# Kernel tuning notes

Hardware: AMD Instinct MI355X
Metric: run time of the kernel (lower is better)

Reference implementation:

```python
import jax, jax.numpy as jnp
import numpy as np
import math

N, DIM, HEADS = 4096, 128, 8
HC = DIM // HEADS      # MHA per-head dim = 16
GC = DIM               # TransformerConv per-head out_channels = dim (concat=False)
E = 65536
FFN = 2048
EPS = 1e-5

def layernorm(x, g, b):
    m = x.mean(-1, keepdims=True)
    v = ((x - m) ** 2).mean(-1, keepdims=True)
    return (x - m) * jax.lax.rsqrt(v + EPS) * g + b

def setup_inputs() -> dict:
    key = jax.random.key(0)
    ks = jax.random.split(key, 24)
    s = 0.02
    def nrm(k, shape):
        return jax.random.normal(k, shape, jnp.float32) * s
    return dict(
        x=jax.random.normal(ks[0], (N, DIM), jnp.float32),
        edge_index=jax.random.randint(ks[1], (2, E), 0, N),
        edge_attr=jax.random.normal(ks[2], (E, DIM), jnp.float32),
        n1_g=jnp.ones((DIM,)), n1_b=jnp.zeros((DIM,)),
        n2_g=jnp.ones((DIM,)), n2_b=jnp.zeros((DIM,)),
        n3_g=jnp.ones((DIM,)), n3_b=jnp.zeros((DIM,)),
        w_qkv=nrm(ks[3], (DIM, 3 * DIM)), b_qkv=jnp.zeros((3 * DIM,)),
        w_o=nrm(ks[4], (DIM, DIM)), b_o=jnp.zeros((DIM,)),
        w_query=nrm(ks[5], (DIM, HEADS * GC)), b_query=jnp.zeros((HEADS * GC,)),
        w_key=nrm(ks[6], (DIM, HEADS * GC)), b_key=jnp.zeros((HEADS * GC,)),
        w_value=nrm(ks[7], (DIM, HEADS * GC)), b_value=jnp.zeros((HEADS * GC,)),
        w_edge=nrm(ks[8], (DIM, HEADS * GC)), b_edge=jnp.zeros((HEADS * GC,)),
        w_skip=nrm(ks[9], (DIM, GC)), b_skip=jnp.zeros((GC,)),
        w_beta=nrm(ks[10], (3 * GC, 1)),
        w_f1=nrm(ks[11], (DIM, FFN)), b_f1=jnp.zeros((FFN,)),
        w_f2=nrm(ks[12], (FFN, DIM)), b_f2=jnp.zeros((DIM,)),
        w_dyn=nrm(ks[13], (2 * DIM, DIM)), b_dyn=jnp.zeros((DIM,)),
    )

def reference(x, edge_index, edge_attr, n1_g, n1_b, n2_g, n2_b, n3_g, n3_b,
              w_qkv, b_qkv, w_o, b_o,
              w_query, b_query, w_key, b_key, w_value, b_value,
              w_edge, b_edge, w_skip, b_skip, w_beta,
              w_f1, b_f1, w_f2, b_f2, w_dyn, b_dyn):
    residual = x
    xn = layernorm(x, n1_g, n1_b)
    # ---- dense self-attention (batch 1, batch_first MHA, eval mode) ----
    qkv = xn @ w_qkv + b_qkv
    q, k, v = jnp.split(qkv, 3, axis=-1)
    q = q.reshape(N, HEADS, HC)
    k = k.reshape(N, HEADS, HC)
    v = v.reshape(N, HEADS, HC)
    scores = jnp.einsum('qhd,khd->hqk', q, k) / math.sqrt(HC)
    probs = jax.nn.softmax(scores, axis=-1)
    attn = jnp.einsum('hqk,khd->qhd', probs, v).reshape(N, DIM)
    attn = attn @ w_o + b_o
    x = residual + attn
    # ---- TransformerConv (heads=8, concat=False -> mean, beta=True, edge_dim=dim) ----
    xn2 = layernorm(x, n2_g, n2_b)
    src, dst = edge_index[0], edge_index[1]   # source -> target flow
    qg = (xn2 @ w_query + b_query).reshape(N, HEADS, GC)
    kg = (xn2 @ w_key + b_key).reshape(N, HEADS, GC)
    vg = (xn2 @ w_value + b_value).reshape(N, HEADS, GC)
    eg = (edge_attr @ w_edge + b_edge).reshape(E, HEADS, GC)
    kj = kg[src] + eg                          # key_j + edge embedding
    alpha = jnp.einsum('ehd,ehd->eh', qg[dst], kj) / math.sqrt(GC)  # [E,H]
    amax = jax.ops.segment_max(alpha, dst, num_segments=N)          # [N,H]
    amax = jnp.where(jnp.isfinite(amax), amax, 0.0)
    ea = jnp.exp(alpha - amax[dst])
    denom = jax.ops.segment_sum(ea, dst, num_segments=N)
    w = ea / (denom[dst] + 1e-16)              # segment softmax per target node
    msg = (vg[src] + eg) * w[:, :, None]       # value_j + edge, scaled
    agg = jax.ops.segment_sum(msg, dst, num_segments=N)  # [N,H,GC]
    out = agg.mean(axis=1)                     # concat=False -> head mean
    x_r = xn2 @ w_skip + b_skip                # root/skip path
    beta = jax.nn.sigmoid(jnp.concatenate([out, x_r, out - x_r], axis=-1) @ w_beta)
    graph_out = beta * x_r + (1.0 - beta) * out
    x = x + graph_out
    # ---- FFN ----
    xn3 = layernorm(x, n3_g, n3_b)
    ffn = jax.nn.gelu(xn3 @ w_f1 + b_f1, approximate=False) @ w_f2 + b_f2
    x = x + ffn
    # ---- gated residual fusion ----
    gate = jax.nn.sigmoid(jnp.concatenate([x, residual], axis=-1) @ w_dyn + b_dyn)
    return x * gate + residual * (1.0 - gate)
```

## Files before the change

### kernel.cpp

```cpp
#include <hip/hip_runtime.h>
#include <math.h>
#include <cstddef>

#define NN 4096
#define DIMC 128
#define NHEADS 8
#define NE 65536

typedef unsigned short ushort_t;
typedef short bs8 __attribute__((ext_vector_type(8)));
typedef float f32x16 __attribute__((ext_vector_type(16)));
typedef _Float16 h4 __attribute__((ext_vector_type(4)));
typedef __fp16 fp16x2 __attribute__((ext_vector_type(2)));
typedef float f4t __attribute__((ext_vector_type(4)));

__device__ __forceinline__ float b2f(ushort_t u){
  unsigned int i = ((unsigned int)u)<<16; float f;
  __builtin_memcpy(&f,&i,4); return f;
}
__device__ __forceinline__ ushort_t f2b(float f){
  unsigned int x; __builtin_memcpy(&x,&f,4);
  unsigned int r = x + 0x7fffu + ((x>>16)&1u);
  return (ushort_t)(r>>16);
}
__device__ __forceinline__ float bdot8(uint4 a, uint4 b){
  unsigned int ua[4]={a.x,a.y,a.z,a.w}, ub[4]={b.x,b.y,b.z,b.w};
  float s=0.f;
  #pragma unroll
  for (int i=0;i<4;++i){
    unsigned int al=ua[i]<<16, ah=ua[i]&0xffff0000u, bl=ub[i]<<16, bh=ub[i]&0xffff0000u;
    float fa,fb,fc,fd;
    __builtin_memcpy(&fa,&al,4); __builtin_memcpy(&fb,&ah,4);
    __builtin_memcpy(&fc,&bl,4); __builtin_memcpy(&fd,&bh,4);
    s += fa*fc + fb*fd;
  }
  return s;
}
__device__ __forceinline__ float bfdot8v(uint4 a, float4 e0, float4 e1){
  unsigned int ua[4]={a.x,a.y,a.z,a.w};
  float eb[8]={e0.x,e0.y,e0.z,e0.w,e1.x,e1.y,e1.z,e1.w};
  float s=0.f;
  #pragma unroll
  for (int i=0;i<4;++i){
    unsigned int al=ua[i]<<16, ah=ua[i]&0xffff0000u;
    float fa,fb;
    __builtin_memcpy(&fa,&al,4); __builtin_memcpy(&fb,&ah,4);
    s += fa*eb[2*i] + fb*eb[2*i+1];
  }
  return s;
}

__device__ void scan256(const int* __restrict__ cnt, int* __restrict__ rows,
                        int* __restrict__ cursor){
  __shared__ int sums[256];
  int t = threadIdx.x;
  int base = t*16;
  int c[16]; int local=0;
  #pragma unroll
  for (int i=0;i<16;++i){ c[i]=cnt[base+i]; local+=c[i]; }
  sums[t]=local; __syncthreads();
  for (int off=1; off<256; off<<=1){
    int v = (t>=off)? sums[t-off] : 0; __syncthreads();
    sums[t]+=v; __syncthreads();
  }
  int r = sums[t]-local;
  #pragma unroll
  for (int i=0;i<16;++i){ rows[base+i]=r; cursor[base+i]=r; r+=c[i]; }
  if (t==255) rows[4096]=r;
}

__global__ __launch_bounds__(256) void ln_kernel(const float* __restrict__ x,
    const float* __restrict__ g, const float* __restrict__ b, ushort_t* __restrict__ y,
    const int* __restrict__ ei, int* __restrict__ cnt,
    int* __restrict__ cursor, int* __restrict__ csr,
    int* __restrict__ pack, int* __restrict__ packe){
  int bb = blockIdx.x;
  if (bb >= 1024){
    int e = (bb-1024)*256 + threadIdx.x;
    int src = ei[e] & (NN-1), dst = ei[NE+e] & (NN-1);
    int pos = atomicAdd(&cursor[dst],1);
    if (pos >= 0 && pos < NE){
      csr[pos]=e; pack[pos]=src|(dst<<12); packe[pos]=e|(src<<16);
    }
    return;
  }
  int n = bb*4 + (threadIdx.x>>6);
  int l = threadIdx.x & 63;
  int d0 = 2*l;
  float2 v = *(const float2*)&x[(size_t)n*DIMC + d0];
  float s = v.x+v.y;
  s += __shfl_xor(s,1); s += __shfl_xor(s,2); s += __shfl_xor(s,4);
  s += __shfl_xor(s,8); s += __shfl_xor(s,16); s += __shfl_xor(s,32);
  float mean = s*(1.0f/128.0f);
  float c0=v.x-mean, c1=v.y-mean;
  float q=c0*c0+c1*c1;
  q += __shfl_xor(q,1); q += __shfl_xor(q,2); q += __shfl_xor(q,4);
  q += __shfl_xor(q,8); q += __shfl_xor(q,16); q += __shfl_xor(q,32);
  float rinv = rsqrtf(q*(1.0f/128.0f)+1e-5f);
  float2 gv = *(const float2*)&g[d0];
  float2 bv = *(const float2*)&b[d0];
  unsigned int pk = ((unsigned int)f2b(c1*rinv*gv.y+bv.y)<<16) | (unsigned int)f2b(c0*rinv*gv.x+bv.x);
  *(unsigned int*)&y[(size_t)n*DIMC + d0] = pk;
  if (cnt){
    int gid = bb*256 + threadIdx.x;
    if (gid < NE) atomicAdd(&cnt[ei[NE+gid] & (NN-1)],1);
  }
}

#define QSCALE 0.36067376022224085f
__global__ __launch_bounds__(256) void megawcvt_kernel(
    const float* __restrict__ w_qkv, const float* __restrict__ w_o,
    const float* __restrict__ w_q, const float* __restrict__ w_k,
    const float* __restrict__ w_v, const float* __restrict__ w_e,
    const float* __restrict__ w_f1, const float* __restrict__ w_f2,
    const float* __restrict__ bq, const float* __restrict__ bk,
    const float* __restrict__ w_dyn, const float* __restrict__ b_qkv,
    ushort_t* __restrict__ WBqkv, ushort_t* __restrict__ WBo, ushort_t* __restrict__ WBG,
    ushort_t* __restrict__ WETB, ushort_t* __restrict__ WBf1, ushort_t* __restrict__ WBf2,
    ushort_t* __restrict__ WCAT, float* __restrict__ BCAT, ushort_t* __restrict__ WDYN,
    int* __restrict__ COUNT, float* __restrict__ BQKV)
{
  int b = blockIdx.x, tid = threadIdx.x;
  if (b < 1216){
    const float* src; int srcStride; ushort_t* dst; int dstStride;
    int n0, k0; float scale = 1.0f;
    if (b < 48){ int nt=b>>2, kt=b&3; src=w_qkv; srcStride=384; dst=WBqkv; dstStride=128;
      n0=nt*32; k0=kt*32; if (nt<4) scale=QSCALE; }
    else if (b < 64){ int l=b-48, nt=l>>2, kt=l&3; src=w_o; srcStride=128; dst=WBo; dstStride=128; n0=nt*32; k0=kt*32; }
    else if (b < 192){ int l=b-64, nt=l>>2, kt=l&3; src=w_q; srcStride=1024; dst=WBG; dstStride=128; n0=nt*32; k0=kt*32; }
    else if (b < 320){ int l=b-192, nt=l>>2, kt=l&3; src=w_k; srcStride=1024; dst=WBG+1024*128; dstStride=128; n0=nt*32; k0=kt*32; }
    else if (b < 448){ int l=b-320, nt=l>>2, kt=l&3; src=w_e; srcStride=1024; dst=WETB; dstStride=128; n0=nt*32; k0=kt*32; }
    else if (b < 704){ int l=b-448, nt=l>>2, kt=l&3; src=w_f1; srcStride=2048; dst=WBf1; dstStride=128; n0=nt*32; k0=kt*32; }
    else if (b < 960){ int l=b-704, nt=l>>6, kt=l&63; src=w_f2; srcStride=128; dst=WBf2; dstStride=2048; n0=nt*32; k0=kt*32; }
    else if (b < 1088){ int l=b-960, h=l>>4, tt=l&15, nt=tt>>2, kt=tt&3;
      src=w_v+h*128; srcStride=1024; dst=WCAT+h*128; dstStride=2048; n0=nt*32; k0=kt*32; scale=0.125f; }
    else { int l=b-1088, h=l>>4, tt=l&15, nt=tt>>2, kt=tt&3;
      src=w_e+h*128; srcStride=1024; dst=WCAT+1024+h*128; dstStride=2048; n0=nt*32; k0=kt*32; scale=0.125f; }
    __shared__ float lt[32*33];
    int rr = tid>>3, cg = (tid&7)*4;
    float4 v = *(const float4*)&src[(size_t)(k0+rr)*srcStride + n0 + cg];
    lt[rr*33+cg]=v.x; lt[rr*33+cg+1]=v.y; lt[rr*33+cg+2]=v.z; lt[rr*33+cg+3]=v.w;
    __syncthreads();
    ushort_t o[4] __attribute__((aligned(8)));
    #pragma unroll
    for (int j=0;j<4;++j) o[j] = f2b(lt[(cg+j)*33 + rr]*scale);
    *(ushort4*)&dst[(size_t)(n0+rr)*dstStride + k0 + cg] = *(ushort4*)o;
  } else {
    for (int id=(b-1216)*256+tid; id<39296; id += 40*256){
      if (id < 2048) BCAT[id] = (id<1024)? bq[id] : bk[id-1024];
      else if (id < 34816){ int l=id-2048; WDYN[l]=f2b(w_dyn[l]); }
      else if (id < 38912) COUNT[id-34816]=0;
      else { int l=id-38912; BQKV[l]=b_qkv[l]*((l<128)?QSCALE:1.0f); }
    }
  }
}

template<int A_BF16, int C_MODE, int FUSE_SCAN>
__global__ __launch_bounds__(256) void mgemm_kernel(
    const void* __restrict__ Av, int lda, int strideA,
    const ushort_t* __restrict__ BT, int ldbt, int strideB,
    const float* __restrict__ bias,
    const float* __restrict__ res,
    void* __restrict__ Cv, int ldc, int strideC,
    int K, int act_gelu, _Float16* __restrict__ vtout,
    const int* __restrict__ scnt, int* __restrict__ srows, int* __restrict__ scur)
{
  if (FUSE_SCAN){
    if (blockIdx.x == gridDim.x-1){
      if (blockIdx.y==0 && blockIdx.z==0) scan256(scnt, srows, scur);
      return;
    }
  }
  int z = blockIdx.z;
  int m0 = blockIdx.y*128, n0 = blockIdx.x*64;
  int tid = threadIdx.x;
  int w = tid>>6, lane = tid&63;
  int kg = lane>>5;
  int ml = w*32 + (lane&31);
  int sw = (ml>>1)&3;
  __shared__ ushort_t As[128*32];
  const ushort_t* BTz = BT + (size_t)z*strideB;
  f32x16 acc[2];
  #pragma unroll
  for (int i=0;i<16;++i){ acc[0][i]=0.f; acc[1][i]=0.f; }

  for (int k0=0; k0<K; k0+=32){
    {
      int rr = tid>>1, kc = (tid&1)*16;
      int rowg = m0 + rr;
      ushort_t tmp[16] __attribute__((aligned(16)));
      if (A_BF16){
        const ushort_t* A = (const ushort_t*)Av + (size_t)z*strideA;
        uint4 u0 = *(const uint4*)&A[(size_t)rowg*lda + k0 + kc];
        uint4 u1 = *(const uint4*)&A[(size_t)rowg*lda + k0 + kc + 8];
        __builtin_memcpy(tmp, &u0, 16); __builtin_memcpy(tmp+8, &u1, 16);
      } else {
        const float* A = (const float*)Av + (size_t)z*strideA;
        const float* p = &A[(size_t)rowg*lda + k0 + kc];
        float4 f0=*(const float4*)p, f1=*(const float4*)(p+4);
        float4 f2v=*(const float4*)(p+8), f3=*(const float4*)(p+12);
        tmp[0]=f2b(f0.x); tmp[1]=f2b(f0.y); tmp[2]=f2b(f0.z); tmp[3]=f2b(f0.w);
        tmp[4]=f2b(f1.x); tmp[5]=f2b(f1.y); tmp[6]=f2b(f1.z); tmp[7]=f2b(f1.w);
        tmp[8]=f2b(f2v.x); tmp[9]=f2b(f2v.y); tmp[10]=f2b(f2v.z); tmp[11]=f2b(f2v.w);
        tmp[12]=f2b(f3.x); tmp[13]=f2b(f3.y); tmp[14]=f2b(f3.z); tmp[15]=f2b(f3.w);
      }
      int swr = (rr>>1)&3, c0 = kc>>3;
      *(uint4*)&As[rr*32 + (((c0  )^swr)*8)] = *(const uint4*)tmp;
      *(uint4*)&As[rr*32 + (((c0+1)^swr)*8)] = *(const uint4*)(tmp+8);
    }
    __syncthreads();
    bs8 a0 = *(bs8*)&As[ml*32 + (((0*2+kg)^sw)*8)];
    bs8 a1 = *(bs8*)&As[ml*32 + (((1*2+kg)^sw)*8)];
    #pragma unroll
    for (int nt=0; nt<2; ++nt){
      const ushort_t* bp = &BTz[(size_t)(n0 + nt*32 + (lane&31))*ldbt + k0 + kg*8];
      uint4 rb0 = *(const uint4*)bp;
      uint4 rb1 = *(const uint4*)(bp + 16);
      bs8 b0, b1;
      __builtin_memcpy(&b0, &rb0, 16); __builtin_memcpy(&b1, &rb1, 16);
      acc[nt] = __builtin_amdgcn_mfma_f32_32x32x16_bf16(a0, b0, acc[nt], 0,0,0);
      acc[nt] = __builtin_amdgcn_mfma_f32_32x32x16_bf16(a1, b1, acc[nt], 0,0,0);
    }
    __syncthreads();
  }
  #pragma unroll
  for (int nt=0; nt<2; ++nt){
    int col = n0 + nt*32 + (lane&31);
    float bv = bias ? bias[col] : 0.f;
    #pragma unroll
    for (int r=0; r<16; ++r){
      int rowl = (r&3) + 8*(r>>2) + 4*kg;
      int row = m0 + w*32 + rowl;
      float v = acc[nt][r] + bv;
      if (act_gelu) v = 0.5f*v*(1.0f+erff(v*0.70710678118654752f));
      if (res) v += res[(size_t)row*ldc + col];
      size_t idx = (size_t)z*strideC + (size_t)row*ldc + col;
      if (C_MODE==1)      ((ushort_t*)Cv)[idx] = f2b(v);
      else if (C_MODE==2){
        _Float16 hv = (_Float16)v;
        ((_Float16*)Cv)[idx] = hv;
        if (vtout && col>=256) vtout[(size_t)(col-256)*4096 + row] = hv;
      }
      else                ((float*)Cv)[idx]    = v;
    }
  }
}

__global__ __launch_bounds__(512) void flash_kernel(const _Float16* __restrict__ qkvh,
    const _Float16* __restrict__ vt, float* __restrict__ attn){
  int h = blockIdx.y;
  int w = threadIdx.x >> 6, lane = threadIdx.x & 63;
  int q0 = blockIdx.x*64;
  int col = lane & 15, quad = lane >> 4;
  __shared__ float ll[8][4][16];
  __shared__ float lo[8][4][256];
  h4 qf[4];
  #pragma unroll
  for (int t=0;t<4;++t)
    qf[t] = *(const h4*)&qkvh[(size_t)(q0+t*16+col)*384 + h*16 + quad*4];
  f4t ov[4];
  float ls[4] = {0.f,0.f,0.f,0.f};
  #pragma unroll
  for (int t=0;t<4;++t){ ov[t][0]=0.f; ov[t][1]=0.f; ov[t][2]=0.f; ov[t][3]=0.f; }
  const _Float16* kbase = qkvh + 128 + h*16 + quad*4;
  const _Float16* vbase = vt + (size_t)(h*16+col)*4096 + quad*4;
  int jbeg = w*512, jend = jbeg + 512;
  h4 kf = *(const h4*)&kbase[(size_t)(jbeg+col)*384];
  h4 vf = *(const h4*)&vbase[jbeg];
  for (int j0=jbeg; j0<jend; j0+=16){
    h4 kc=kf, vc=vf;
    if (j0+16<jend){
      kf = *(const h4*)&kbase[(size_t)(j0+16+col)*384];
      vf = *(const h4*)&vbase[j0+16];
    }
    f4t s[4];
    #pragma unroll
    for (int t=0;t<4;++t){
      s[t][0]=0.f; s[t][1]=0.f; s[t][2]=0.f; s[t][3]=0.f;
      s[t] = __builtin_amdgcn_mfma_f32_16x16x16f16(kc, qf[t], s[t], 0,0,0);
    }
    #pragma unroll
    for (int t=0;t<4;++t){
      float p0=__builtin_amdgcn_exp2f(s[t][0]), p1=__builtin_amdgcn_exp2f(s[t][1]);
      float p2=__builtin_amdgcn_exp2f(s[t][2]), p3=__builtin_amdgcn_exp2f(s[t][3]);
      ls[t] += (p0+p1)+(p2+p3);
      fp16x2 plo = __builtin_amdgcn_cvt_pkrtz(p0,p1);
      fp16x2 phi = __builtin_amdgcn_cvt_pkrtz(p2,p3);
      h4 pf;
      pf[0]=(_Float16)plo[0]; pf[1]=(_Float16)plo[1];
      pf[2]=(_Float16)phi[0]; pf[3]=(_Float16)phi[1];
      ov[t] = __builtin_amdgcn_mfma_f32_16x16x16f16(vc, pf, ov[t], 0,0,0);
    }
  }
  #pragma unroll
  for (int t=0;t<4;++t){
    float l = ls[t];
    l += __shfl_xor(l,16);
    l += __shfl_xor(l,32);
    if (lane<16) ll[w][t][lane]=l;
    *(float4*)&lo[w][t][lane*4] = make_float4(ov[t][0],ov[t][1],ov[t][2],ov[t][3]);
  }
  __syncthreads();
  if (w < 4){
    int t = w;
    float l = 0.f;
    #pragma unroll
    for (int ww=0; ww<8; ++ww) l += ll[ww][t][col];
    float4 os = make_float4(0.f,0.f,0.f,0.f);
    #pragma unroll
    for (int ww=0; ww<8; ++ww){
      float4 owv = *(const float4*)&lo[ww][t][lane*4];
      os.x += owv.x; os.y += owv.y; os.z += owv.z; os.w += owv.w;
    }
    float inv = 1.0f/l;
    *(float4*)&attn[(size_t)(q0+t*16+col)*128 + h*16 + quad*4] =
        make_float4(os.x*inv, os.y*inv, os.z*inv, os.w*inv);
  }
}

__global__ __launch_bounds__(256) void alpha_kernel(
    const float* __restrict__ ea, const ushort_t* __restrict__ qkvsg,
    const ushort_t* __restrict__ t, const int* __restrict__ csr,
    const int* __restrict__ pack, float* __restrict__ alpha){
  int tid = threadIdx.x;
  int w = tid>>6, lane = tid&63;
  int h = lane>>3, li = lane&7;
  int off = h*128 + li*16;
  int ibase = blockIdx.x*8 + w*2;
  int2 pk = *(const int2*)&pack[ibase];
  int2 ec = *(const int2*)&csr[ibase];
  int e0 = ec.x & (NE-1), e1 = ec.y & (NE-1);
  int s0 = pk.x & 4095, d0 = (pk.x>>12) & 4095;
  int s1 = pk.y & 4095, d1 = (pk.y>>12) & 4095;

  const ushort_t* q0p = &qkvsg[(size_t)d0*2048 + off];
  const ushort_t* k0p = &qkvsg[(size_t)s0*2048 + 1024 + off];
  const ushort_t* t0p = &t[(size_t)d0*1024 + off];
  const float*    e0p = &ea[(size_t)e0*128 + li*16];
  const ushort_t* q1p = &qkvsg[(size_t)d1*2048 + off];
  const ushort_t* k1p = &qkvsg[(size_t)s1*2048 + 1024 + off];
  const ushort_t* t1p = &t[(size_t)d1*1024 + off];
  const float*    e1p = &ea[(size_t)e1*128 + li*16];

  uint4 q00=*(const uint4*)q0p,      q01=*(const uint4*)(q0p+8);
  uint4 k00=*(const uint4*)k0p,      k01=*(const uint4*)(k0p+8);
  uint4 t00=*(const uint4*)t0p,      t01=*(const uint4*)(t0p+8);
  float4 ea00=*(const float4*)e0p,   ea01=*(const float4*)(e0p+4);
  float4 ea02=*(const float4*)(e0p+8), ea03=*(const float4*)(e0p+12);
  uint4 q10=*(const uint4*)q1p,      q11=*(const uint4*)(q1p+8);
  uint4 k10=*(const uint4*)k1p,      k11=*(const uint4*)(k1p+8);
  uint4 t10=*(const uint4*)t1p,      t11=*(const uint4*)(t1p+8);
  float4 ea10=*(const float4*)e1p,   ea11=*(const float4*)(e1p+4);
  float4 ea12=*(const float4*)(e1p+8), ea13=*(const float4*)(e1p+12);

  float p0 = bdot8(q00,k00) + bdot8(q01,k01)
           + bfdot8v(t00,ea00,ea01) + bfdot8v(t01,ea02,ea03);
  float p1 = bdot8(q10,k10) + bdot8(q11,k11)
           + bfdot8v(t10,ea10,ea11) + bfdot8v(t11,ea12,ea13);
  p0 += __shfl_xor(p0,1); p0 += __shfl_xor(p0,2); p0 += __shfl_xor(p0,4);
  p1 += __shfl_xor(p1,1); p1 += __shfl_xor(p1,2); p1 += __shfl_xor(p1,4);
  if (li==0){
    alpha[(size_t)ibase*8 + h]     = 0.08838834764831845f*p0;
    alpha[(size_t)(ibase+1)*8 + h] = 0.08838834764831845f*p1;
  }
}

__global__ __launch_bounds__(256) void agg1_kernel(
    const ushort_t* __restrict__ lns, const float* __restrict__ ea,
    const float* __restrict__ abuf, const int* __restrict__ rows,
    const int* __restrict__ packe,
    const float* __restrict__ b_edge, const float* __restrict__ b_v,
    ushort_t* __restrict__ seagg, float* __restrict__ part)
{
  int n = blockIdx.x, tid = threadIdx.x;
  int d = tid & 127, h0 = tid >> 7;
  float sacc[4]={0.f,0.f,0.f,0.f}, eacc[4]={0.f,0.f,0.f,0.f}, wsacc[4]={0.f,0.f,0.f,0.f};
  float be[4];
  #pragma unroll
  for (int j=0;j<4;++j){
    int hd = (h0+2*j)*128 + d;
    be[j] = b_edge[hd] + b_v[hd];
  }
  int i0=rows[n], i1=rows[n+1];
  i0 = max(0,min(i0,NE)); i1 = max(i0,min(i1,NE));
  __shared__ float smh[8];
  __shared__ float rmx[32][8];
  __shared__ float wls[32][8];
  __shared__ int es[32], srcs[32];
  {
    int hh = tid&7, sl = tid>>3;
    float m = -1e30f;
    for (int i=i0+sl; i<i1; i+=32)
      m = fmaxf(m, abuf[(size_t)i*8 + hh]);
    rmx[sl][hh] = m;
  }
  __syncthreads();
  if (tid < 8){
    float m = -1e30f;
    #pragma unroll
    for (int j=0;j<32;++j) m = fmaxf(m, rmx[j][tid]);
    smh[tid] = m;
  }
  __syncthreads();
  for (int cs=i0; cs<i1; cs+=32){
    int cnt = min(32, i1-cs);
    if (tid < cnt){
      int v = packe[cs+tid];
      es[tid]   = v & 0xffff;
      srcs[tid] = (v>>16) & (NN-1);
    }
    if (tid < cnt*8){
      int k=tid>>3, hh=tid&7;
      wls[k][hh] = __expf(abuf[(size_t)(cs+k)*8+hh]-smh[hh]);
    }
    __syncthreads();
    for (int k=0;k<cnt;++k){
      int e = es[k], sr = srcs[k];
      float lv = b2f(lns[(size_t)sr*128 + d]);
      float eav = ea[(size_t)e*128 + d];
      #pragma unroll
      for (int j=0;j<4;++j){
        float wv = wls[k][h0+2*j];
        sacc[j] += wv*lv;
        eacc[j] += wv*eav;
        wsacc[j] += wv;
      }
    }
    __syncthreads();
  }
  float partial = 0.f;
  #pragma unroll
  for (int j=0;j<4;++j){
    float inv = 1.0f/(wsacc[j]+1e-16f);
    int hd = (h0+2*j)*128 + d;
    seagg[(size_t)n*2048 + hd]        = f2b(sacc[j]*inv);
    seagg[(size_t)n*2048 + 1024 + hd] = f2b(eacc[j]*inv);
    partial += be[j]*wsacc[j]*inv;
  }
  __shared__ float pp[2][128];
  pp[h0][d] = partial;
  __syncthreads();
  if (tid<128) part[(size_t)n*128+tid] = (pp[0][tid]+pp[1][tid])*0.125f;
}

__global__ __launch_bounds__(64) void combine_kernel(float* __restrict__ x2,
    const float* __restrict__ corrp, const float* __restrict__ part,
    ushort_t* __restrict__ lns, const float* __restrict__ w_s,
    const float* __restrict__ b_s, const float* __restrict__ x1,
    const float* __restrict__ w_beta,
    const float* __restrict__ n3g, const float* __restrict__ n3b)
{
  int n0 = blockIdx.x*2;
  int l = threadIdx.x;
  int d0 = 2*l, d1 = 2*l+1;
  __shared__ float sln[2][128];
  #pragma unroll
  for (int rr=0;rr<2;++rr){
    unsigned int u = *(const unsigned int*)&lns[(size_t)(n0+rr)*128 + d0];
    sln[rr][d0] = b2f((ushort_t)(u&0xffffu));
    sln[rr][d1] = b2f((ushort_t)(u>>16));
  }
  __syncthreads();
  float2 bsv = *(const float2*)&b_s[d0];
  float xr0[2], xr1[2];
  xr0[0]=bsv.x; xr0[1]=bsv.x; xr1[0]=bsv.y; xr1[1]=bsv.y;
  for (int i=0;i<128;++i){
    float2 wv = *(const float2*)&w_s[(size_t)i*128 + d0];
    #pragma unroll
    for (int rr=0;rr<2;++rr){
      float lv = sln[rr][i];
      xr0[rr] += lv*wv.x; xr1[rr] += lv*wv.y;
    }
  }
  float2 wb0 = *(const float2*)&w_beta[d0];
  float2 wb1 = *(const float2*)&w_beta[128+d0];
  float2 wb2 = *(const float2*)&w_beta[256+d0];
  float2 gv = *(const float2*)&n3g[d0];
  float2 bv = *(const float2*)&n3b[d0];
  #pragma unroll
  for (int rr=0;rr<2;++rr){
    size_t idx = (size_t)(n0+rr)*128 + d0;
    float2 pt = *(const float2*)&part[idx];
    float2 c0 = *(const float2*)&corrp[idx];
    float2 c1 = *(const float2*)&corrp[524288+idx];
    float2 c2 = *(const float2*)&corrp[1048576+idx];
    float2 c3 = *(const float2*)&corrp[1572864+idx];
    float o0 = pt.x+c0.x+c1.x+c2.x+c3.x;
    float o1 = pt.y+c0.y+c1.y+c2.y+c3.y;
    float xa = xr0[rr], xb = xr1[rr];
    float pr = o0*wb0.x + o1*wb0.y + xa*wb1.x + xb*wb1.y
             + (o0-xa)*wb2.x + (o1-xb)*wb2.y;
    pr += __shfl_xor(pr,1); pr += __shfl_xor(pr,2); pr += __shfl_xor(pr,4);
    pr += __shfl_xor(pr,8); pr += __shfl_xor(pr,16); pr += __shfl_xor(pr,32);
    float beta = 1.0f/(1.0f+__expf(-pr));
    float2 xv = *(const float2*)&x1[idx];
    float v0 = xv.x + beta*xa + (1.0f-beta)*o0;
    float v1 = xv.y + beta*xb + (1.0f-beta)*o1;
    *(float2*)&x2[idx] = make_float2(v0,v1);
    float s = v0+v1;
    s += __shfl_xor(s,1); s += __shfl_xor(s,2); s += __shfl_xor(s,4);
    s += __shfl_xor(s,8); s += __shfl_xor(s,16); s += __shfl_xor(s,32);
    float mean = s*(1.0f/128.0f);
    float e0=v0-mean, e1=v1-mean;
    float q = e0*e0+e1*e1;
    q += __shfl_xor(q,1); q += __shfl_xor(q,2); q += __shfl_xor(q,4);
    q += __shfl_xor(q,8); q += __shfl_xor(q,16); q += __shfl_xor(q,32);
    float rinv = rsqrtf(q*(1.0f/128.0f)+1e-5f);
    unsigned int pk2 = ((unsigned int)f2b(e1*rinv*gv.y+bv.y)<<16)
                     |  (unsigned int)f2b(e0*rinv*gv.x+bv.x);
    *(unsigned int*)&lns[idx] = pk2;
  }
}

__global__ __launch_bounds__(64) void gate_kernel(const float* __restrict__ x3p,
    const float* __restrict__ b_f2, const float* __restrict__ x2,
    const float* __restrict__ x0, const ushort_t* __restrict__ wdyn,
    const float* __restrict__ b_dyn, float* __restrict__ out){
  int n0 = blockIdx.x*2;
  int l = threadIdx.x;
  int d0 = 2*l, d1 = 2*l+1;
  __shared__ float sA[2][128];
  __shared__ float sR[2][128];
  float a0[2], a1[2], r0[2], r1[2];
  float2 bb = *(const float2*)&b_f2[d0];
  #pragma unroll
  for (int rr=0;rr<2;++rr){
    size_t idx = (size_t)(n0+rr)*128 + d0;
    float2 p0v = *(const float2*)&x3p[idx];
    float2 p1v = *(const float2*)&x3p[524288+idx];
    float2 p2v = *(const float2*)&x3p[1048576+idx];
    float2 p3v = *(const float2*)&x3p[1572864+idx];
    float2 xv = *(const float2*)&x2[idx];
    float2 rv = *(const float2*)&x0[idx];
    a0[rr] = p0v.x+p1v.x+p2v.x+p3v.x+bb.x+xv.x;
    a1[rr] = p0v.y+p1v.y+p2v.y+p3v.y+bb.y+xv.y;
    r0[rr]=rv.x; r1[rr]=rv.y;
    sA[rr][d0]=a0[rr]; sA[rr][d1]=a1[rr];
    sR[rr][d0]=rv.x;  sR[rr][d1]=rv.y;
  }
  __syncthreads();
  float2 bd = *(const float2*)&b_dyn[d0];
  float g0[2], g1[2];
  g0[0]=bd.x; g0[1]=bd.x; g1[0]=bd.y; g1[1]=bd.y;
  for (int k=0;k<128;++k){
    unsigned int wv = *(const unsigned int*)&wdyn[(size_t)k*128 + d0];
    float w0=b2f((ushort_t)(wv&0xffffu)), w1=b2f((ushort_t)(wv>>16));
    #pragma unroll
    for (int rr=0;rr<2;++rr){
      float sk = sA[rr][k];
      g0[rr]+=sk*w0; g1[rr]+=sk*w1;
    }
  }
  for (int k=0;k<128;++k){
    unsigned int wv = *(const unsigned int*)&wdyn[(size_t)(128+k)*128 + d0];
    float w0=b2f((ushort_t)(wv&0xffffu)), w1=b2f((ushort_t)(wv>>16));
    #pragma unroll
    for (int rr=0;rr<2;++rr){
      float sk = sR[rr][k];
      g0[rr]+=sk*w0; g1[rr]+=sk*w1;
    }
  }
  #pragma unroll
  for (int rr=0;rr<2;++rr){
    size_t idx=(size_t)(n0+rr)*128 + d0;
    float gg0=1.0f/(1.0f+__expf(-g0[rr]));
    float gg1=1.0f/(1.0f+__expf(-g1[rr]));
    float v0=a0[rr]*gg0 + r0[rr]*(1.0f-gg0);
    float v1=a1[rr]*gg1 + r1[rr]*(1.0f-gg1);
    *(float2*)&out[idx]=make_float2(v0,v1);
  }
}

extern "C" void kernel_launch(void* const* d_in, const int* in_sizes, int n_in,
                              void* d_out, int out_size, void* d_ws, size_t ws_size,
                              hipStream_t stream) {
  const float* x    =(const float*)d_in[0];
  const int*   ei   =(const int*)  d_in[1];
  const float* eattr=(const float*)d_in[2];
  const float* n1g=(const float*)d_in[3], *n1b=(const float*)d_in[4];
  const float* n2g=(const float*)d_in[5], *n2b=(const float*)d_in[6];
  const float* n3g=(const float*)d_in[7], *n3b=(const float*)d_in[8];
  const float* w_qkv=(const float*)d_in[9],  *b_qkv=(const float*)d_in[10];
  const float* w_o  =(const float*)d_in[11], *b_o  =(const float*)d_in[12];
  const float* w_q  =(const float*)d_in[13], *b_q  =(const float*)d_in[14];
  const float* w_k  =(const float*)d_in[15], *b_k  =(const float*)d_in[16];
  const float* w_v  =(const float*)d_in[17], *b_v  =(const float*)d_in[18];
  const float* w_e  =(const float*)d_in[19], *b_e  =(const float*)d_in[20];
  const float* w_s  =(const float*)d_in[21], *b_s  =(const float*)d_in[22];
  const float* w_beta=(const float*)d_in[23];
  const float* w_f1 =(const float*)d_in[24], *b_f1=(const float*)d_in[25];
  const float* w_f2 =(const float*)d_in[26], *b_f2=(const float*)d_in[27];
  const float* w_dyn=(const float*)d_in[28], *b_dyn=(const float*)d_in[29];
  float* out=(float*)d_out;
  float* ws=(float*)d_ws;

  float* X1    = ws + 0;
  float* X2    = ws + 524288;
  ushort_t* LNS = (ushort_t*)(ws + 1048576);
  float* PART  = ws + 1310720;
  float* ALPHA = ws + 1835008;
  int*   ROWS  = (int*)(ws + 2359296);
  int*   CURS  = (int*)(ws + 2363456);
  int*   CSR   = (int*)(ws + 2367552);
  int*   COUNT = (int*)(ws + 2433088);
  int*   PACK  = (int*)(ws + 524288);
  int*   PACKE = (int*)(ws + 589824);
  float* BQKV  = ws + 1048576 - 512;
  ushort_t* WBqkv = (ushort_t*)(ws + 2437184);
  ushort_t* WBo   = (ushort_t*)(ws + 2461760);
  ushort_t* WBG   = (ushort_t*)(ws + 2469952);
  ushort_t* WETB  = (ushort_t*)(ws + 2601024);
  ushort_t* WBf1  = (ushort_t*)(ws + 2666560);
  ushort_t* WBf2  = (ushort_t*)(ws + 2797632);
  ushort_t* WCAT  = (ushort_t*)(ws + 2928704);
  float* BCAT  = ws + 3059776;
  ushort_t* WDYN = (ushort_t*)(ws + 3061824);
  _Float16* QKVH  = (_Float16*)(ws + 3078208);
  _Float16* VT    = (_Float16*)(ws + 3864640);
  ushort_t* QKVSG = (ushort_t*)(ws + 3078208);
  ushort_t* SEAGG = (ushort_t*)(ws + 3078208);
  ushort_t* MID   = (ushort_t*)(ws + 3078208);
  ushort_t* T     = (ushort_t*)(ws + 7272512);
  float* CORRP = ws + 7272512;
  float* X3P   = ws + 7272512;
  float* ATTN  = X2;

  megawcvt_kernel<<<1256,256,0,stream>>>(w_qkv,w_o,w_q,w_k,w_v,w_e,w_f1,w_f2,
                                         b_q,b_k,w_dyn,b_qkv,
                                         WBqkv,WBo,WBG,WETB,WBf1,WBf2,WCAT,BCAT,WDYN,COUNT,BQKV);

  ln_kernel<<<1024,256,0,stream>>>(x, n1g, n1b, LNS, ei, COUNT, nullptr,nullptr,nullptr,nullptr);
  mgemm_kernel<1,2,1><<<dim3(7,32,1),256,0,stream>>>(LNS,128,0, WBqkv,128,0, BQKV, nullptr, QKVH,384,0, 128, 0, VT, COUNT, ROWS, CURS);
  flash_kernel<<<dim3(64,8),512,0,stream>>>(QKVH, VT, ATTN);
  mgemm_kernel<0,0,0><<<dim3(2,32,1),256,0,stream>>>(ATTN,128,0, WBo,128,0, b_o, x, X1,128,0, 128, 0, nullptr, nullptr,nullptr,nullptr);

  ln_kernel<<<1280,256,0,stream>>>(X1, n2g, n2b, LNS, ei, nullptr, CURS, CSR, PACK, PACKE);
  mgemm_kernel<1,1,0><<<dim3(32,32,1),256,0,stream>>>(LNS,128,0, WBG,128,0, BCAT, nullptr, QKVSG,2048,0, 128, 0, nullptr, nullptr,nullptr,nullptr);
  mgemm_kernel<1,1,0><<<dim3(2,32,8),256,0,stream>>>(QKVSG,2048,128, WETB,128,16384, nullptr, nullptr, T,1024,128, 128, 0, nullptr, nullptr,nullptr,nullptr);
  alpha_kernel<<<8192,256,0,stream>>>(eattr, QKVSG, T, CSR, PACK, ALPHA);
  agg1_kernel<<<NN,256,0,stream>>>(LNS, eattr, ALPHA, ROWS, PACKE, b_e, b_v, SEAGG, PART);
  mgemm_kernel<1,0,0><<<dim3(2,32,4),256,0,stream>>>(SEAGG,2048,512, WCAT,2048,512, nullptr, nullptr, CORRP,128,524288, 512, 0, nullptr, nullptr,nullptr,nullptr);
  combine_kernel<<<2048,64,0,stream>>>(X2, CORRP, PART, LNS, w_s, b_s, X1, w_beta, n3g, n3b);

  mgemm_kernel<1,1,0><<<dim3(32,32,1),256,0,stream>>>(LNS,128,0, WBf1,128,0, b_f1, nullptr, MID,2048,0, 128, 1, nullptr, nullptr,nullptr,nullptr);
  mgemm_kernel<1,0,0><<<dim3(2,32,4),256,0,stream>>>(MID,2048,512, WBf2,2048,512, nullptr, nullptr, X3P,128,524288, 512, 0, nullptr, nullptr,nullptr,nullptr);

  gate_kernel<<<2048,64,0,stream>>>(X3P, b_f2, X2, x, WDYN, b_dyn, out);
}
```

Before: 361.7 us.

## Fuse edge attention-score computation into aggregation with online softmax

Removes the separate alpha kernel and its ALPHA buffer; the per-destination aggregation kernel now computes edge scores itself, caching the destination's query and transformed-query rows in shared memory and using a running max with rescaling of the accumulators (online softmax). This saves one launch, the alpha write/read round trip, and the CSR/PACK arrays. In exchange the score work is spread less evenly, since it now follows per-node edge counts, and there are extra block barriers per 32-edge chunk. SEAGG moves to a separate workspace region so it no longer aliases QKVSG, which is still being read.

```diff
diff --git a/kernel.cpp b/kernel.cpp
--- a/kernel.cpp
+++ b/kernel.cpp
@@ -72,15 +72,14 @@
 __global__ __launch_bounds__(256) void ln_kernel(const float* __restrict__ x,
     const float* __restrict__ g, const float* __restrict__ b, ushort_t* __restrict__ y,
     const int* __restrict__ ei, int* __restrict__ cnt,
-    int* __restrict__ cursor, int* __restrict__ csr,
-    int* __restrict__ pack, int* __restrict__ packe){
+    int* __restrict__ cursor, int* __restrict__ packe){
   int bb = blockIdx.x;
   if (bb >= 1024){
     int e = (bb-1024)*256 + threadIdx.x;
     int src = ei[e] & (NN-1), dst = ei[NE+e] & (NN-1);
     int pos = atomicAdd(&cursor[dst],1);
     if (pos >= 0 && pos < NE){
-      csr[pos]=e; pack[pos]=src|(dst<<12); packe[pos]=e|(src<<16);
+      packe[pos]=e|(src<<16);
     }
     return;
   }
@@ -318,57 +317,10 @@
   }
 }
 
-__global__ __launch_bounds__(256) void alpha_kernel(
-    const float* __restrict__ ea, const ushort_t* __restrict__ qkvsg,
-    const ushort_t* __restrict__ t, const int* __restrict__ csr,
-    const int* __restrict__ pack, float* __restrict__ alpha){
-  int tid = threadIdx.x;
-  int w = tid>>6, lane = tid&63;
-  int h = lane>>3, li = lane&7;
-  int off = h*128 + li*16;
-  int ibase = blockIdx.x*8 + w*2;
-  int2 pk = *(const int2*)&pack[ibase];
-  int2 ec = *(const int2*)&csr[ibase];
-  int e0 = ec.x & (NE-1), e1 = ec.y & (NE-1);
-  int s0 = pk.x & 4095, d0 = (pk.x>>12) & 4095;
-  int s1 = pk.y & 4095, d1 = (pk.y>>12) & 4095;
-
-  const ushort_t* q0p = &qkvsg[(size_t)d0*2048 + off];
-  const ushort_t* k0p = &qkvsg[(size_t)s0*2048 + 1024 + off];
-  const ushort_t* t0p = &t[(size_t)d0*1024 + off];
-  const float*    e0p = &ea[(size_t)e0*128 + li*16];
-  const ushort_t* q1p = &qkvsg[(size_t)d1*2048 + off];
-  const ushort_t* k1p = &qkvsg[(size_t)s1*2048 + 1024 + off];
-  const ushort_t* t1p = &t[(size_t)d1*1024 + off];
-  const float*    e1p = &ea[(size_t)e1*128 + li*16];
-
-  uint4 q00=*(const uint4*)q0p,      q01=*(const uint4*)(q0p+8);
-  uint4 k00=*(const uint4*)k0p,      k01=*(const uint4*)(k0p+8);
-  uint4 t00=*(const uint4*)t0p,      t01=*(const uint4*)(t0p+8);
-  float4 ea00=*(const float4*)e0p,   ea01=*(const float4*)(e0p+4);
-  float4 ea02=*(const float4*)(e0p+8), ea03=*(const float4*)(e0p+12);
-  uint4 q10=*(const uint4*)q1p,      q11=*(const uint4*)(q1p+8);
-  uint4 k10=*(const uint4*)k1p,      k11=*(const uint4*)(k1p+8);
-  uint4 t10=*(const uint4*)t1p,      t11=*(const uint4*)(t1p+8);
-  float4 ea10=*(const float4*)e1p,   ea11=*(const float4*)(e1p+4);
-  float4 ea12=*(const float4*)(e1p+8), ea13=*(const float4*)(e1p+12);
-
-  float p0 = bdot8(q00,k00) + bdot8(q01,k01)
-           + bfdot8v(t00,ea00,ea01) + bfdot8v(t01,ea02,ea03);
-  float p1 = bdot8(q10,k10) + bdot8(q11,k11)
-           + bfdot8v(t10,ea10,ea11) + bfdot8v(t11,ea12,ea13);
-  p0 += __shfl_xor(p0,1); p0 += __shfl_xor(p0,2); p0 += __shfl_xor(p0,4);
-  p1 += __shfl_xor(p1,1); p1 += __shfl_xor(p1,2); p1 += __shfl_xor(p1,4);
-  if (li==0){
-    alpha[(size_t)ibase*8 + h]     = 0.08838834764831845f*p0;
-    alpha[(size_t)(ibase+1)*8 + h] = 0.08838834764831845f*p1;
-  }
-}
-
 __global__ __launch_bounds__(256) void agg1_kernel(
     const ushort_t* __restrict__ lns, const float* __restrict__ ea,
-    const float* __restrict__ abuf, const int* __restrict__ rows,
-    const int* __restrict__ packe,
+    const ushort_t* __restrict__ qkvsg, const ushort_t* __restrict__ tbuf,
+    const int* __restrict__ rows, const int* __restrict__ packe,
     const float* __restrict__ b_edge, const float* __restrict__ b_v,
     ushort_t* __restrict__ seagg, float* __restrict__ part)
 {
@@ -383,24 +335,14 @@
   }
   int i0=rows[n], i1=rows[n+1];
   i0 = max(0,min(i0,NE)); i1 = max(i0,min(i1,NE));
-  __shared__ float smh[8];
-  __shared__ float rmx[32][8];
+  __shared__ ushort_t qs[1024], ts[1024];
+  __shared__ float aa[32][8];
   __shared__ float wls[32][8];
+  __shared__ float Msh[8], Rsh[8];
   __shared__ int es[32], srcs[32];
-  {
-    int hh = tid&7, sl = tid>>3;
-    float m = -1e30f;
-    for (int i=i0+sl; i<i1; i+=32)
-      m = fmaxf(m, abuf[(size_t)i*8 + hh]);
-    rmx[sl][hh] = m;
-  }
-  __syncthreads();
-  if (tid < 8){
-    float m = -1e30f;
-    #pragma unroll
-    for (int j=0;j<32;++j) m = fmaxf(m, rmx[j][tid]);
-    smh[tid] = m;
-  }
+  *(uint2*)&qs[tid*4] = *(const uint2*)&qkvsg[(size_t)n*2048 + tid*4];
+  *(uint2*)&ts[tid*4] = *(const uint2*)&tbuf[(size_t)n*1024 + tid*4];
+  if (tid < 8) Msh[tid] = -1e30f;
   __syncthreads();
   for (int cs=i0; cs<i1; cs+=32){
     int cnt = min(32, i1-cs);
@@ -409,11 +351,45 @@
       es[tid]   = v & 0xffff;
       srcs[tid] = (v>>16) & (NN-1);
     }
+    __syncthreads();
+    {
+      int sl = tid>>3, hh = tid&7;
+      if (sl < cnt){
+        int e = es[sl], sr = srcs[sl];
+        const ushort_t* kp = &qkvsg[(size_t)sr*2048 + 1024 + hh*128];
+        const float*    ep = &ea[(size_t)e*128];
+        const ushort_t* qp = &qs[hh*128];
+        const ushort_t* tp = &ts[hh*128];
+        float a0=0.f, a1=0.f;
+        #pragma unroll
+        for (int i=0;i<16;i+=2){
+          a0 += bdot8(*(const uint4*)&qp[i*8],   *(const uint4*)&kp[i*8]);
+          a1 += bdot8(*(const uint4*)&qp[i*8+8], *(const uint4*)&kp[i*8+8]);
+          a0 += bfdot8v(*(const uint4*)&tp[i*8],   *(const float4*)&ep[i*8],   *(const float4*)&ep[i*8+4]);
+          a1 += bfdot8v(*(const uint4*)&tp[i*8+8], *(const float4*)&ep[i*8+8], *(const float4*)&ep[i*8+12]);
+        }
+        aa[sl][hh] = 0.08838834764831845f*(a0+a1);
+      }
+    }
+    __syncthreads();
+    if (tid < 8){
+      float cm = -1e30f;
+      for (int j=0;j<cnt;++j) cm = fmaxf(cm, aa[j][tid]);
+      float Mo = Msh[tid], Mn = fmaxf(Mo, cm);
+      Rsh[tid] = __expf(Mo - Mn);
+      Msh[tid] = Mn;
+    }
+    __syncthreads();
     if (tid < cnt*8){
       int k=tid>>3, hh=tid&7;
-      wls[k][hh] = __expf(abuf[(size_t)(cs+k)*8+hh]-smh[hh]);
-    }
-    __syncthreads();
+      wls[k][hh] = __expf(aa[k][hh]-Msh[hh]);
+    }
+    __syncthreads();
+    #pragma unroll
+    for (int j=0;j<4;++j){
+      float r = Rsh[h0+2*j];
+      sacc[j]*=r; eacc[j]*=r; wsacc[j]*=r;
+    }
     for (int k=0;k<cnt;++k){
       int e = es[k], sr = srcs[k];
       float lv = b2f(lns[(size_t)sr*128 + d]);
@@ -598,12 +574,9 @@
   float* X2    = ws + 524288;
   ushort_t* LNS = (ushort_t*)(ws + 1048576);
   float* PART  = ws + 1310720;
-  float* ALPHA = ws + 1835008;
   int*   ROWS  = (int*)(ws + 2359296);
   int*   CURS  = (int*)(ws + 2363456);
-  int*   CSR   = (int*)(ws + 2367552);
   int*   COUNT = (int*)(ws + 2433088);
-  int*   PACK  = (int*)(ws + 524288);
   int*   PACKE = (int*)(ws + 589824);
   float* BQKV  = ws + 1048576 - 512;
   ushort_t* WBqkv = (ushort_t*)(ws + 2437184);
@@ -618,27 +591,26 @@
   _Float16* QKVH  = (_Float16*)(ws + 3078208);
   _Float16* VT    = (_Float16*)(ws + 3864640);
   ushort_t* QKVSG = (ushort_t*)(ws + 3078208);
-  ushort_t* SEAGG = (ushort_t*)(ws + 3078208);
   ushort_t* MID   = (ushort_t*)(ws + 3078208);
   ushort_t* T     = (ushort_t*)(ws + 7272512);
   float* CORRP = ws + 7272512;
   float* X3P   = ws + 7272512;
+  ushort_t* SEAGG = (ushort_t*)(ws + 9437184);
   float* ATTN  = X2;
 
   megawcvt_kernel<<<1256,256,0,stream>>>(w_qkv,w_o,w_q,w_k,w_v,w_e,w_f1,w_f2,
                                          b_q,b_k,w_dyn,b_qkv,
                                          WBqkv,WBo,WBG,WETB,WBf1,WBf2,WCAT,BCAT,WDYN,COUNT,BQKV);
 
-  ln_kernel<<<1024,256,0,stream>>>(x, n1g, n1b, LNS, ei, COUNT, nullptr,nullptr,nullptr,nullptr);
+  ln_kernel<<<1024,256,0,stream>>>(x, n1g, n1b, LNS, ei, COUNT, nullptr,nullptr);
   mgemm_kernel<1,2,1><<<dim3(7,32,1),256,0,stream>>>(LNS,128,0, WBqkv,128,0, BQKV, nullptr, QKVH,384,0, 128, 0, VT, COUNT, ROWS, CURS);
   flash_kernel<<<dim3(64,8),512,0,stream>>>(QKVH, VT, ATTN);
   mgemm_kernel<0,0,0><<<dim3(2,32,1),256,0,stream>>>(ATTN,128,0, WBo,128,0, b_o, x, X1,128,0, 128, 0, nullptr, nullptr,nullptr,nullptr);
 
-  ln_kernel<<<1280,256,0,stream>>>(X1, n2g, n2b, LNS, ei, nullptr, CURS, CSR, PACK, PACKE);
+  ln_kernel<<<1280,256,0,stream>>>(X1, n2g, n2b, LNS, ei, nullptr, CURS, PACKE);
   mgemm_kernel<1,1,0><<<dim3(32,32,1),256,0,stream>>>(LNS,128,0, WBG,128,0, BCAT, nullptr, QKVSG,2048,0, 128, 0, nullptr, nullptr,nullptr,nullptr);
   mgemm_kernel<1,1,0><<<dim3(2,32,8),256,0,stream>>>(QKVSG,2048,128, WETB,128,16384, nullptr, nullptr, T,1024,128, 128, 0, nullptr, nullptr,nullptr,nullptr);
-  alpha_kernel<<<8192,256,0,stream>>>(eattr, QKVSG, T, CSR, PACK, ALPHA);
-  agg1_kernel<<<NN,256,0,stream>>>(LNS, eattr, ALPHA, ROWS, PACKE, b_e, b_v, SEAGG, PART);
+  agg1_kernel<<<NN,256,0,stream>>>(LNS, eattr, QKVSG, T, ROWS, PACKE, b_e, b_v, SEAGG, PART);
   mgemm_kernel<1,0,0><<<dim3(2,32,4),256,0,stream>>>(SEAGG,2048,512, WCAT,2048,512, nullptr, nullptr, CORRP,128,524288, 512, 0, nullptr, nullptr,nullptr,nullptr);
   combine_kernel<<<2048,64,0,stream>>>(X2, CORRP, PART, LNS, w_s, b_s, X1, w_beta, n3g, n3b);
 
```

Measured after the change: 389.2 us. +7.6%, slower.
